# Kernel optimization log

Hardware: AMD Instinct MI355X
Metric: run time of the kernel (lower is better)

## Reference

```python
import jax, jax.numpy as jnp
import numpy as np


def _hard_sigmoid(x):
    # Keras ConvLSTM2D default recurrent_activation
    return jnp.clip(0.2 * x + 0.5, 0.0, 1.0)


def _conv(x, w):
    # NHWC input, HWIO kernel, SAME padding, stride 1
    return jax.lax.conv_general_dilated(
        x, w, (1, 1), 'SAME', dimension_numbers=('NHWC', 'HWIO', 'NHWC'))


def _convlstm(seq, h, c, k, rk, b):
    # seq: [B, T, H, W, Cin]; h, c: [B, H, W, F]
    # k: [kh, kw, Cin, 4F], rk: [kh, kw, F, 4F], b: [4F]
    def step(carry, x):
        h, c = carry
        z = _conv(x, k) + _conv(h, rk) + b  # [B,H,W,4F]
        zi, zf, zc, zo = jnp.split(z, 4, axis=-1)
        i = _hard_sigmoid(zi)
        f = _hard_sigmoid(zf)
        o = _hard_sigmoid(zo)
        c = f * c + i * jnp.tanh(zc)
        h = o * jnp.tanh(c)
        return (h, c), None
    (h, c), _ = jax.lax.scan(step, (h, c), jnp.swapaxes(seq, 0, 1))
    return h, c


def setup_inputs() -> dict:
    key = jax.random.key(0)
    ks = jax.random.split(key, 14)
    B, T, H, W, Cin, F, K = 32, 1, 64, 64, 1, 64, 3
    s = 0.05
    inp = {
        'input_': jax.random.normal(ks[0], (B, T, H, W, Cin), jnp.float32),
        'h0': jax.random.normal(ks[1], (B, H, W, F), jnp.float32) * s,
        'c0': jax.random.normal(ks[2], (B, H, W, F), jnp.float32) * s,
        'h1': jax.random.normal(ks[3], (B, H, W, F), jnp.float32) * s,
        'c1': jax.random.normal(ks[4], (B, H, W, F), jnp.float32) * s,
        'k0': jax.random.normal(ks[5], (K, K, Cin, 4 * F), jnp.float32) * s,
        'rk0': jax.random.normal(ks[6], (K, K, F, 4 * F), jnp.float32) * s,
        'b0': jnp.zeros((4 * F,), jnp.float32),
        'k1': jax.random.normal(ks[7], (K, K, F, 4 * F), jnp.float32) * s,
        'rk1': jax.random.normal(ks[8], (K, K, F, 4 * F), jnp.float32) * s,
        'b1': jnp.zeros((4 * F,), jnp.float32),
        'cw': jax.random.normal(ks[9], (1, 1, F, 1), jnp.float32) * s,
        'cb': jnp.zeros((1,), jnp.float32),
    }
    return inp


def reference(input_, h0, c0, h1, c1, k0, rk0, b0, k1, rk1, b1, cw, cb):
    # Layer 0 consumes the input frame sequence (T=1)
    h0n, c0n = _convlstm(input_, h0, c0, k0, rk0, b0)
    # Layer 1 consumes layer-0's last hidden state as its (length-1) input
    h1n, c1n = _convlstm(h0n[:, None], h1, c1, k1, rk1, b1)
    frames = _conv(h1n, cw) + cb  # 1x1 conv head -> [B,H,W,1]
    return frames, h0n, c0n, h1n, c1n
```

## Files before the change

### kernel.cpp

```cpp
#include <hip/hip_runtime.h>
#include <hip/hip_bf16.h>

typedef short s16;
typedef __attribute__((ext_vector_type(8))) short bf16x8;
typedef __attribute__((ext_vector_type(4))) float f32x4;

__device__ __forceinline__ s16 f2bf(float f) {
  unsigned u = __builtin_bit_cast(unsigned, f);
  unsigned r = (u + 0x7FFFu + ((u >> 16) & 1u)) >> 16;
  return (s16)r;
}

__device__ __forceinline__ float hsig(float x) {
  return fminf(fmaxf(0.2f * x + 0.5f, 0.0f), 1.0f);
}

#define PXS 66
#define ROWSZ (PXS * 64)
#define ASZ4 (4 * ROWSZ)
#define ASZ6 (6 * ROWSZ)

__global__ void wprep_kernel(const float* __restrict__ rk0, const float* __restrict__ k1,
                             const float* __restrict__ rk1, const float* __restrict__ k0,
                             s16* __restrict__ w0q, s16* __restrict__ w1q,
                             s16* __restrict__ w2q, s16* __restrict__ k0t) {
  int idx = blockIdx.x * 256 + threadIdx.x;
  const int n1 = 18 * 8192;
  if (idx < 3 * n1) {
    int which = idx / n1;
    int i = idx - which * n1;
    int e    = i & 7;
    int lane = (i >> 3) & 63;
    int g    = (i >> 9) & 3;
    int j    = (i >> 11) & 3;
    int k    = (i >> 13) & 1;
    int tap  = i >> 14;
    int l15 = lane & 15, l4 = lane >> 4;
    int ic = k * 32 + l4 * 8 + e;
    int oc = j * 64 + g * 16 + l15;
    const float* src = (which == 0) ? rk0 : (which == 1) ? k1 : rk1;
    s16* dst = (which == 0) ? w0q : (which == 1) ? w1q : w2q;
    dst[i] = f2bf(src[(tap * 64 + ic) * 256 + oc]);
  } else if (idx < 3 * n1 + 8192) {
    int r = idx - 3 * n1;
    int kk = r & 31;
    int oc = r >> 5;
    k0t[r] = (kk < 9) ? f2bf(k0[kk * 256 + oc]) : (s16)0;
  }
}

template <bool F32>
__device__ __forceinline__ bf16x8 load_conv8(const void* src, long off) {
  if constexpr (F32) {
    const float* p = (const float*)src + off;
    float4 v0 = *reinterpret_cast<const float4*>(p);
    float4 v1 = *reinterpret_cast<const float4*>(p + 4);
    bf16x8 r;
    r[0] = f2bf(v0.x); r[1] = f2bf(v0.y); r[2] = f2bf(v0.z); r[3] = f2bf(v0.w);
    r[4] = f2bf(v1.x); r[5] = f2bf(v1.y); r[6] = f2bf(v1.z); r[7] = f2bf(v1.w);
    return r;
  } else {
    return *reinterpret_cast<const bf16x8*>((const s16*)src + off);
  }
}

template <bool F32, int ROWS, int NT>
__device__ __forceinline__ void stageA(s16* a_lds, const void* src, int b, int y0, int tid) {
  #pragma unroll
  for (int i = 0; i < ROWS * 512 / NT; ++i) {
    int c   = tid + i * NT;
    int row = c >> 9;
    int px  = (c >> 3) & 63;
    int cb  = c & 7;
    int y   = y0 - 1 + row;
    int xp  = px + 1;
    bf16x8 v = {};
    if ((unsigned)y < 64u)
      v = load_conv8<F32>(src, ((long)(b * 64 + y) * 64 + px) * 64 + cb * 8);
    *reinterpret_cast<bf16x8*>(a_lds + (row * PXS + xp) * 64 + ((cb ^ (xp & 7)) * 8)) = v;
  }
  if (tid < ROWS * 16) {
    int row = tid >> 4;
    int xp  = ((tid >> 3) & 1) ? 65 : 0;
    int cb  = tid & 7;
    bf16x8 z = {};
    *reinterpret_cast<bf16x8*>(a_lds + (row * PXS + xp) * 64 + cb * 8) = z;
  }
}

__global__ __launch_bounds__(1024, 4) void cell0_kernel(
    const float* __restrict__ h0,
    const s16* __restrict__ w0,
    const float* __restrict__ xin,
    const s16* __restrict__ k0t,
    const float* __restrict__ bias,
    const float* __restrict__ c_old,
    float* __restrict__ h_out,
    float* __restrict__ c_out,
    s16* __restrict__ hb_out)
{
  __shared__ __align__(16) s16 a_lds[ASZ4];
  __shared__ __align__(16) s16 w_lds[4][8192];
  __shared__ float x_lds[256];

  const int tid = threadIdx.x;
  const int b  = blockIdx.x >> 5;
  const int y0 = (blockIdx.x & 31) << 1;

  const int wave = tid >> 6;
  const int lane = tid & 63;
  const int g    = wave & 3;
  const int mq   = wave >> 2;
  const int l15  = lane & 15;
  const int l4   = lane >> 4;

  constexpr int NST = 18;

  auto issueW = [&](int u) {
    int v = (u >= NST) ? u - NST : u;
    const s16* wt = w0 + v * 8192;
    char* base = (char*)(&w_lds[0][0]) + (u & 3) * 16384 + (tid >> 6) * 1024;
    __builtin_amdgcn_global_load_lds(
        (const __attribute__((address_space(1))) void*)(wt + tid * 8),
        (__attribute__((address_space(3))) void*)base, 16, 0, 0);
  };
  auto readWf = [&](bf16x8 (&wf)[4], int u) {
    const s16* wb = &w_lds[u & 3][0] + g * 512 + lane * 8;
    #pragma unroll
    for (int j = 0; j < 4; ++j)
      wf[j] = *reinterpret_cast<const bf16x8*>(wb + j * 2048);
  };
  auto readA = [&](bf16x8 (&af)[2], int u) {
    int v = (u >= NST) ? u - NST : u;
    int tap = v >> 1, kk = v & 1;
    int dy = tap / 3, dx = tap - dy * 3;
    const char* sb = (const char*)a_lds + ((mq >> 1) + dy) * (ROWSZ * 2);
    #pragma unroll
    for (int m = 0; m < 2; ++m) {
      int xq   = (mq & 1) * 32 + m * 16 + l15 + dx;
      int boff = xq * 128 + ((((kk << 2) | l4) ^ (xq & 7)) << 4);
      af[m] = *reinterpret_cast<const bf16x8*>(sb + boff);
    }
  };

  f32x4 acc[2][4] = {};

  auto doMfma = [&](const bf16x8 (&af)[2], const bf16x8 (&wf)[4]) {
    __builtin_amdgcn_s_setprio(1);
    #pragma unroll
    for (int m = 0; m < 2; ++m) {
      #pragma unroll
      for (int j = 0; j < 4; ++j)
        acc[m][j] = __builtin_amdgcn_mfma_f32_16x16x32_bf16(af[m], wf[j], acc[m][j], 0, 0, 0);
    }
    __builtin_amdgcn_s_setprio(0);
  };

  issueW(0);
  issueW(1);
  issueW(2);
  stageA<true, 4, 1024>(a_lds, h0, b, y0, tid);
  if (tid < 256) {
    int row = tid >> 6, px = tid & 63;
    int y = y0 - 1 + row;
    x_lds[tid] = ((unsigned)y < 64u) ? xin[(b * 64 + y) * 64 + px] : 0.0f;
  }
  __syncthreads();

  {
    const int rb = mq >> 1;
    #pragma unroll
    for (int m = 0; m < 2; ++m) {
      int px = (mq & 1) * 32 + m * 16 + l15;
      bf16x8 ax = {};
      #pragma unroll
      for (int e = 0; e < 8; ++e) {
        int t = l4 * 8 + e;
        if (t < 9) {
          int dyt = t / 3, dxt = t - dyt * 3;
          int xx = px + dxt - 1;
          float xv = ((unsigned)xx < 64u) ? x_lds[(rb + dyt) * 64 + xx] : 0.0f;
          ax[e] = f2bf(xv);
        }
      }
      #pragma unroll
      for (int j = 0; j < 4; ++j) {
        int oc = j * 64 + g * 16 + l15;
        bf16x8 bx = *reinterpret_cast<const bf16x8*>(k0t + oc * 32 + l4 * 8);
        acc[m][j] = __builtin_amdgcn_mfma_f32_16x16x32_bf16(ax, bx, acc[m][j], 0, 0, 0);
      }
    }
  }

  bf16x8 afA[2], afB[2], wfA[4], wfB[4];
  readA(afA, 0);
  readWf(wfA, 0);
  #pragma unroll
  for (int u = 0; u < NST; u += 2) {
    asm volatile("s_waitcnt vmcnt(1)" ::: "memory");
    __builtin_amdgcn_s_barrier();
    issueW(u + 3);
    readA(afB, u + 1);
    readWf(wfB, u + 1);
    doMfma(afA, wfA);
    asm volatile("s_waitcnt vmcnt(1)" ::: "memory");
    __builtin_amdgcn_s_barrier();
    issueW(u + 4);
    readA(afA, u + 2);
    readWf(wfA, u + 2);
    doMfma(afB, wfB);
  }

  float bi[4];
  #pragma unroll
  for (int j = 0; j < 4; ++j) bi[j] = bias[j * 64 + g * 16 + l15];
  const int pix_base = b * 4096 + y0 * 64;
  const int f = g * 16 + l15;
  #pragma unroll
  for (int m = 0; m < 2; ++m) {
    #pragma unroll
    for (int r = 0; r < 4; ++r) {
      int pl = mq * 32 + m * 16 + l4 * 4 + r;
      int off = (pix_base + pl) * 64 + f;
      float zi = acc[m][0][r] + bi[0];
      float zf = acc[m][1][r] + bi[1];
      float zc = acc[m][2][r] + bi[2];
      float zo = acc[m][3][r] + bi[3];
      float ig = hsig(zi), fg = hsig(zf), og = hsig(zo);
      float cn = fg * c_old[off] + ig * tanhf(zc);
      float hn = og * tanhf(cn);
      c_out[off] = cn;
      h_out[off] = hn;
      hb_out[off] = f2bf(hn);
    }
  }
}

__global__ __launch_bounds__(512, 2) void cell1_kernel(
    const s16* __restrict__ src0,
    const float* __restrict__ src1,
    const s16* __restrict__ w0,
    const s16* __restrict__ w1,
    const float* __restrict__ bias,
    const float* __restrict__ c_old,
    float* __restrict__ h_out,
    float* __restrict__ c_out)
{
  __shared__ __align__(16) s16 a_lds[2 * ASZ6];
  __shared__ __align__(16) s16 w_lds[3][8192];

  const int tid = threadIdx.x;
  const int b  = blockIdx.x >> 4;
  const int y0 = (blockIdx.x & 15) << 2;

  const int wave = tid >> 6;
  const int lane = tid & 63;
  const int g    = wave & 3;
  const int mh   = wave >> 2;
  const int l15  = lane & 15;
  const int l4   = lane >> 4;

  constexpr int NST = 36;

  auto issueW = [&](int u) {
    int v = (u >= NST) ? u - NST : u;
    int si = (v >= 18) ? 1 : 0;
    const s16* wt = (si ? w1 : w0) + (v - 18 * si) * 8192;
    char* sl = (char*)(&w_lds[0][0]) + (u % 3) * 16384 + wave * 1024;
    __builtin_amdgcn_global_load_lds(
        (const __attribute__((address_space(1))) void*)(wt + wave * 512 + lane * 8),
        (__attribute__((address_space(3))) void*)sl, 16, 0, 0);
    __builtin_amdgcn_global_load_lds(
        (const __attribute__((address_space(1))) void*)(wt + 4096 + wave * 512 + lane * 8),
        (__attribute__((address_space(3))) void*)(sl + 8192), 16, 0, 0);
  };

  auto readWf = [&](bf16x8 (&wf)[4], int u) {
    const s16* wb = &w_lds[0][0] + (u % 3) * 8192 + g * 512 + lane * 8;
    #pragma unroll
    for (int j = 0; j < 4; ++j)
      wf[j] = *reinterpret_cast<const bf16x8*>(wb + j * 2048);
  };

  f32x4 acc[8][4] = {};

  auto doStage = [&](const bf16x8 (&wf)[4], int u) {
    int si = (u >= 18) ? 1 : 0;
    int uu = u - 18 * si;
    int tap = uu >> 1, kk = uu & 1;
    int dy = tap / 3, dx = tap - dy * 3;
    const char* sb = (const char*)a_lds + si * (ASZ6 * 2);
    bf16x8 af[8];
    #pragma unroll
    for (int m = 0; m < 8; ++m) {
      int row  = 2 * mh + (m >> 2) + dy;
      int xq   = (m & 3) * 16 + l15 + dx;
      int boff = xq * 128 + ((((kk << 2) | l4) ^ (xq & 7)) << 4);
      af[m] = *reinterpret_cast<const bf16x8*>(sb + row * (ROWSZ * 2) + boff);
    }
    __builtin_amdgcn_s_setprio(1);
    #pragma unroll
    for (int m = 0; m < 8; ++m) {
      #pragma unroll
      for (int j = 0; j < 4; ++j)
        acc[m][j] = __builtin_amdgcn_mfma_f32_16x16x32_bf16(af[m], wf[j], acc[m][j], 0, 0, 0);
    }
    __builtin_amdgcn_s_setprio(0);
  };

  issueW(0);
  issueW(1);
  stageA<false, 6, 512>(a_lds, src0, b, y0, tid);
  stageA<true, 6, 512>(a_lds + ASZ6, src1, b, y0, tid);
  __syncthreads();

  bf16x8 wfA[4], wfB[4];
  readWf(wfA, 0);
  #pragma unroll
  for (int u = 0; u < NST; u += 2) {
    asm volatile("s_waitcnt vmcnt(0)" ::: "memory");
    __builtin_amdgcn_s_barrier();
    issueW(u + 2);
    readWf(wfB, u + 1);
    doStage(wfA, u);
    asm volatile("s_waitcnt vmcnt(0)" ::: "memory");
    __builtin_amdgcn_s_barrier();
    issueW(u + 3);
    readWf(wfA, (u + 2 < NST) ? u + 2 : 0);
    doStage(wfB, u + 1);
  }

  float bi[4];
  #pragma unroll
  for (int j = 0; j < 4; ++j) bi[j] = bias[j * 64 + g * 16 + l15];
  const int pix_base = b * 4096 + y0 * 64;
  const int f = g * 16 + l15;
  #pragma unroll
  for (int m = 0; m < 8; ++m) {
    #pragma unroll
    for (int r = 0; r < 4; ++r) {
      int pl = (2 * mh + (m >> 2)) * 64 + (m & 3) * 16 + l4 * 4 + r;
      int off = (pix_base + pl) * 64 + f;
      float zi = acc[m][0][r] + bi[0];
      float zf = acc[m][1][r] + bi[1];
      float zc = acc[m][2][r] + bi[2];
      float zo = acc[m][3][r] + bi[3];
      float ig = hsig(zi), fg = hsig(zf), og = hsig(zo);
      float cn = fg * c_old[off] + ig * tanhf(zc);
      float hn = og * tanhf(cn);
      c_out[off] = cn;
      h_out[off] = hn;
    }
  }
}

__global__ void frames_kernel(const float* __restrict__ h, const float* __restrict__ cw,
                              const float* __restrict__ cbp, float* __restrict__ out) {
  int tid = blockIdx.x * 256 + threadIdx.x;
  int p  = tid >> 2;
  int fc = (tid & 3) * 16;
  const float4* hp = reinterpret_cast<const float4*>(h + p * 64 + fc);
  const float4* wp = reinterpret_cast<const float4*>(cw + fc);
  float s = 0.0f;
  #pragma unroll
  for (int i = 0; i < 4; ++i) {
    float4 v = hp[i];
    float4 w = wp[i];
    s += v.x * w.x + v.y * w.y + v.z * w.z + v.w * w.w;
  }
  s += __shfl_xor(s, 1);
  s += __shfl_xor(s, 2);
  if ((tid & 3) == 0) out[p] = s + cbp[0];
}

extern "C" void kernel_launch(void* const* d_in, const int* in_sizes, int n_in,
                              void* d_out, int out_size, void* d_ws, size_t ws_size,
                              hipStream_t stream) {
  const float* x   = (const float*)d_in[0];
  const float* h0  = (const float*)d_in[1];
  const float* c0  = (const float*)d_in[2];
  const float* h1  = (const float*)d_in[3];
  const float* c1  = (const float*)d_in[4];
  const float* k0  = (const float*)d_in[5];
  const float* rk0 = (const float*)d_in[6];
  const float* b0  = (const float*)d_in[7];
  const float* k1  = (const float*)d_in[8];
  const float* rk1 = (const float*)d_in[9];
  const float* b1  = (const float*)d_in[10];
  const float* cw  = (const float*)d_in[11];
  const float* cbp = (const float*)d_in[12];

  float* out    = (float*)d_out;
  float* frames = out;
  float* h0n    = out + 131072;
  float* c0n    = out + 131072 + 8388608;
  float* h1n    = out + 131072 + 2 * 8388608;
  float* c1n    = out + 131072 + 3 * 8388608;

  char* ws = (char*)d_ws;
  const size_t SZ_H = 16777216;
  s16* h0nb = (s16*)(ws + 0 * SZ_H);
  s16* w0q  = (s16*)(ws + 1 * SZ_H);
  s16* w1q  = (s16*)(ws + 1 * SZ_H + 1 * 294912);
  s16* w2q  = (s16*)(ws + 1 * SZ_H + 2 * 294912);
  s16* k0t  = (s16*)(ws + 1 * SZ_H + 3 * 294912);

  wprep_kernel<<<1760, 256, 0, stream>>>(rk0, k1, rk1, k0, w0q, w1q, w2q, k0t);

  cell0_kernel<<<1024, 1024, 0, stream>>>(
      h0, w0q, x, k0t, b0, c0, h0n, c0n, h0nb);

  cell1_kernel<<<512, 512, 0, stream>>>(
      h0nb, h1, w1q, w2q, b1, c1, h1n, c1n);

  frames_kernel<<<2048, 256, 0, stream>>>(h1n, cw, cbp, frames);
}
```

Before: 202.6 us.

## Swap tile shapes between cell0 and cell1 kernels

Cell0 now processes four output rows per block with 512 blocks and a 3-slot weight ring, loading each weight stage once per larger tile. Cell1 switches to two rows per 1024-thread block with 1024 blocks and a 4-slot ring, trading weight reuse for more parallelism and occupancy. The goal is to rebalance per-kernel reuse against occupancy. In exchange, cell0 loads more redundant halo rows per block and cell1 refetches its weights from global memory twice as often.

```diff
diff --git a/kernel.cpp b/kernel.cpp
--- a/kernel.cpp
+++ b/kernel.cpp
@@ -88,7 +88,7 @@
   }
 }
 
-__global__ __launch_bounds__(1024, 4) void cell0_kernel(
+__global__ __launch_bounds__(1024, 1) void cell0_kernel(
     const float* __restrict__ h0,
     const s16* __restrict__ w0,
     const float* __restrict__ xin,
@@ -99,18 +99,18 @@
     float* __restrict__ c_out,
     s16* __restrict__ hb_out)
 {
-  __shared__ __align__(16) s16 a_lds[ASZ4];
-  __shared__ __align__(16) s16 w_lds[4][8192];
-  __shared__ float x_lds[256];
+  __shared__ __align__(16) s16 a_lds[ASZ6];
+  __shared__ __align__(16) s16 w_lds[3][8192];
+  __shared__ float x_lds[384];
 
   const int tid = threadIdx.x;
-  const int b  = blockIdx.x >> 5;
-  const int y0 = (blockIdx.x & 31) << 1;
+  const int b  = blockIdx.x >> 4;
+  const int y0 = (blockIdx.x & 15) << 2;
 
   const int wave = tid >> 6;
   const int lane = tid & 63;
   const int g    = wave & 3;
-  const int mq   = wave >> 2;
+  const int mh   = wave >> 2;
   const int l15  = lane & 15;
   const int l4   = lane >> 4;
 
@@ -119,36 +119,34 @@
   auto issueW = [&](int u) {
     int v = (u >= NST) ? u - NST : u;
     const s16* wt = w0 + v * 8192;
-    char* base = (char*)(&w_lds[0][0]) + (u & 3) * 16384 + (tid >> 6) * 1024;
+    char* base = (char*)(&w_lds[0][0]) + (v % 3) * 16384 + (tid >> 6) * 1024;
     __builtin_amdgcn_global_load_lds(
         (const __attribute__((address_space(1))) void*)(wt + tid * 8),
         (__attribute__((address_space(3))) void*)base, 16, 0, 0);
   };
-  auto readWf = [&](bf16x8 (&wf)[4], int u) {
-    const s16* wb = &w_lds[u & 3][0] + g * 512 + lane * 8;
+  auto readWf = [&](bf16x8 (&wf)[4], int slot) {
+    const s16* wb = &w_lds[slot][0] + g * 512 + lane * 8;
     #pragma unroll
     for (int j = 0; j < 4; ++j)
       wf[j] = *reinterpret_cast<const bf16x8*>(wb + j * 2048);
   };
-  auto readA = [&](bf16x8 (&af)[2], int u) {
-    int v = (u >= NST) ? u - NST : u;
-    int tap = v >> 1, kk = v & 1;
+
+  f32x4 acc[4][4] = {};
+
+  auto doStage = [&](const bf16x8 (&wf)[4], int u) {
+    int tap = u >> 1, kk = u & 1;
     int dy = tap / 3, dx = tap - dy * 3;
-    const char* sb = (const char*)a_lds + ((mq >> 1) + dy) * (ROWSZ * 2);
-    #pragma unroll
-    for (int m = 0; m < 2; ++m) {
-      int xq   = (mq & 1) * 32 + m * 16 + l15 + dx;
+    const char* sb = (const char*)a_lds + (mh + dy) * (ROWSZ * 2);
+    bf16x8 af[4];
+    #pragma unroll
+    for (int m = 0; m < 4; ++m) {
+      int xq   = m * 16 + l15 + dx;
       int boff = xq * 128 + ((((kk << 2) | l4) ^ (xq & 7)) << 4);
       af[m] = *reinterpret_cast<const bf16x8*>(sb + boff);
     }
-  };
-
-  f32x4 acc[2][4] = {};
-
-  auto doMfma = [&](const bf16x8 (&af)[2], const bf16x8 (&wf)[4]) {
     __builtin_amdgcn_s_setprio(1);
     #pragma unroll
-    for (int m = 0; m < 2; ++m) {
+    for (int m = 0; m < 4; ++m) {
       #pragma unroll
       for (int j = 0; j < 4; ++j)
         acc[m][j] = __builtin_amdgcn_mfma_f32_16x16x32_bf16(af[m], wf[j], acc[m][j], 0, 0, 0);
@@ -158,9 +156,8 @@
 
   issueW(0);
   issueW(1);
-  issueW(2);
-  stageA<true, 4, 1024>(a_lds, h0, b, y0, tid);
-  if (tid < 256) {
+  stageA<true, 6, 1024>(a_lds, h0, b, y0, tid);
+  if (tid < 384) {
     int row = tid >> 6, px = tid & 63;
     int y = y0 - 1 + row;
     x_lds[tid] = ((unsigned)y < 64u) ? xin[(b * 64 + y) * 64 + px] : 0.0f;
@@ -168,10 +165,15 @@
   __syncthreads();
 
   {
-    const int rb = mq >> 1;
-    #pragma unroll
-    for (int m = 0; m < 2; ++m) {
-      int px = (mq & 1) * 32 + m * 16 + l15;
+    bf16x8 bx[4];
+    #pragma unroll
+    for (int j = 0; j < 4; ++j) {
+      int oc = j * 64 + g * 16 + l15;
+      bx[j] = *reinterpret_cast<const bf16x8*>(k0t + oc * 32 + l4 * 8);
+    }
+    #pragma unroll
+    for (int m = 0; m < 4; ++m) {
+      int px = m * 16 + l15;
       bf16x8 ax = {};
       #pragma unroll
       for (int e = 0; e < 8; ++e) {
@@ -179,18 +181,129 @@
         if (t < 9) {
           int dyt = t / 3, dxt = t - dyt * 3;
           int xx = px + dxt - 1;
-          float xv = ((unsigned)xx < 64u) ? x_lds[(rb + dyt) * 64 + xx] : 0.0f;
+          float xv = ((unsigned)xx < 64u) ? x_lds[(mh + dyt) * 64 + xx] : 0.0f;
           ax[e] = f2bf(xv);
         }
       }
       #pragma unroll
-      for (int j = 0; j < 4; ++j) {
-        int oc = j * 64 + g * 16 + l15;
-        bf16x8 bx = *reinterpret_cast<const bf16x8*>(k0t + oc * 32 + l4 * 8);
-        acc[m][j] = __builtin_amdgcn_mfma_f32_16x16x32_bf16(ax, bx, acc[m][j], 0, 0, 0);
-      }
-    }
-  }
+      for (int j = 0; j < 4; ++j)
+        acc[m][j] = __builtin_amdgcn_mfma_f32_16x16x32_bf16(ax, bx[j], acc[m][j], 0, 0, 0);
+    }
+  }
+
+  bf16x8 wf[4];
+  #pragma unroll
+  for (int u = 0; u < NST; ++u) {
+    asm volatile("s_waitcnt vmcnt(1)" ::: "memory");
+    __builtin_amdgcn_s_barrier();
+    __builtin_amdgcn_sched_barrier(0);
+    issueW(u + 2);
+    readWf(wf, u % 3);
+    doStage(wf, u);
+  }
+
+  float bi[4];
+  #pragma unroll
+  for (int j = 0; j < 4; ++j) bi[j] = bias[j * 64 + g * 16 + l15];
+  const int pix_base = b * 4096 + y0 * 64;
+  const int f = g * 16 + l15;
+  #pragma unroll
+  for (int m = 0; m < 4; ++m) {
+    #pragma unroll
+    for (int r = 0; r < 4; ++r) {
+      int pl = mh * 64 + m * 16 + l4 * 4 + r;
+      int off = (pix_base + pl) * 64 + f;
+      float zi = acc[m][0][r] + bi[0];
+      float zf = acc[m][1][r] + bi[1];
+      float zc = acc[m][2][r] + bi[2];
+      float zo = acc[m][3][r] + bi[3];
+      float ig = hsig(zi), fg = hsig(zf), og = hsig(zo);
+      float cn = fg * c_old[off] + ig * tanhf(zc);
+      float hn = og * tanhf(cn);
+      c_out[off] = cn;
+      h_out[off] = hn;
+      hb_out[off] = f2bf(hn);
+    }
+  }
+}
+
+__global__ __launch_bounds__(1024, 4) void cell1_kernel(
+    const s16* __restrict__ src0,
+    const float* __restrict__ src1,
+    const s16* __restrict__ w0,
+    const s16* __restrict__ w1,
+    const float* __restrict__ bias,
+    const float* __restrict__ c_old,
+    float* __restrict__ h_out,
+    float* __restrict__ c_out)
+{
+  __shared__ __align__(16) s16 a_lds[2 * ASZ4];
+  __shared__ __align__(16) s16 w_lds[4][8192];
+
+  const int tid = threadIdx.x;
+  const int b  = blockIdx.x >> 5;
+  const int y0 = (blockIdx.x & 31) << 1;
+
+  const int wave = tid >> 6;
+  const int lane = tid & 63;
+  const int g    = wave & 3;
+  const int mq   = wave >> 2;
+  const int l15  = lane & 15;
+  const int l4   = lane >> 4;
+
+  constexpr int NST = 36;
+
+  auto issueW = [&](int u) {
+    int v = (u >= NST) ? u - NST : u;
+    int si = (v >= 18) ? 1 : 0;
+    const s16* wt = (si ? w1 : w0) + (v - 18 * si) * 8192;
+    char* base = (char*)(&w_lds[0][0]) + (u & 3) * 16384 + (tid >> 6) * 1024;
+    __builtin_amdgcn_global_load_lds(
+        (const __attribute__((address_space(1))) void*)(wt + tid * 8),
+        (__attribute__((address_space(3))) void*)base, 16, 0, 0);
+  };
+
+  auto readWf = [&](bf16x8 (&wf)[4], int u) {
+    const s16* wb = &w_lds[u & 3][0] + g * 512 + lane * 8;
+    #pragma unroll
+    for (int j = 0; j < 4; ++j)
+      wf[j] = *reinterpret_cast<const bf16x8*>(wb + j * 2048);
+  };
+
+  auto readA = [&](bf16x8 (&af)[2], int u) {
+    int v = (u >= NST) ? u - NST : u;
+    int si = (v >= 18) ? 1 : 0;
+    int uu = v - 18 * si;
+    int tap = uu >> 1, kk = uu & 1;
+    int dy = tap / 3, dx = tap - dy * 3;
+    const char* sb = (const char*)a_lds + si * (ASZ4 * 2) + ((mq >> 1) + dy) * (ROWSZ * 2);
+    #pragma unroll
+    for (int m = 0; m < 2; ++m) {
+      int xq   = (mq & 1) * 32 + m * 16 + l15 + dx;
+      int boff = xq * 128 + ((((kk << 2) | l4) ^ (xq & 7)) << 4);
+      af[m] = *reinterpret_cast<const bf16x8*>(sb + boff);
+    }
+  };
+
+  f32x4 acc[2][4] = {};
+
+  auto doMfma = [&](const bf16x8 (&af)[2], const bf16x8 (&wf)[4]) {
+    __builtin_amdgcn_s_setprio(1);
+    #pragma unroll
+    for (int m = 0; m < 2; ++m) {
+      #pragma unroll
+      for (int j = 0; j < 4; ++j)
+        acc[m][j] = __builtin_amdgcn_mfma_f32_16x16x32_bf16(af[m], wf[j], acc[m][j], 0, 0, 0);
+    }
+    __builtin_amdgcn_s_setprio(0);
+  };
+
+  issueW(0);
+  issueW(1);
+  issueW(2);
+  stageA<false, 4, 1024>(a_lds, src0, b, y0, tid);
+  stageA<true, 4, 1024>(a_lds + ASZ4, src1, b, y0, tid);
+  __syncthreads();
 
   bf16x8 afA[2], afB[2], wfA[4], wfB[4];
   readA(afA, 0);
@@ -221,125 +334,6 @@
     #pragma unroll
     for (int r = 0; r < 4; ++r) {
       int pl = mq * 32 + m * 16 + l4 * 4 + r;
-      int off = (pix_base + pl) * 64 + f;
-      float zi = acc[m][0][r] + bi[0];
-      float zf = acc[m][1][r] + bi[1];
-      float zc = acc[m][2][r] + bi[2];
-      float zo = acc[m][3][r] + bi[3];
-      float ig = hsig(zi), fg = hsig(zf), og = hsig(zo);
-      float cn = fg * c_old[off] + ig * tanhf(zc);
-      float hn = og * tanhf(cn);
-      c_out[off] = cn;
-      h_out[off] = hn;
-      hb_out[off] = f2bf(hn);
-    }
-  }
-}
-
-__global__ __launch_bounds__(512, 2) void cell1_kernel(
-    const s16* __restrict__ src0,
-    const float* __restrict__ src1,
-    const s16* __restrict__ w0,
-    const s16* __restrict__ w1,
-    const float* __restrict__ bias,
-    const float* __restrict__ c_old,
-    float* __restrict__ h_out,
-    float* __restrict__ c_out)
-{
-  __shared__ __align__(16) s16 a_lds[2 * ASZ6];
-  __shared__ __align__(16) s16 w_lds[3][8192];
-
-  const int tid = threadIdx.x;
-  const int b  = blockIdx.x >> 4;
-  const int y0 = (blockIdx.x & 15) << 2;
-
-  const int wave = tid >> 6;
-  const int lane = tid & 63;
-  const int g    = wave & 3;
-  const int mh   = wave >> 2;
-  const int l15  = lane & 15;
-  const int l4   = lane >> 4;
-
-  constexpr int NST = 36;
-
-  auto issueW = [&](int u) {
-    int v = (u >= NST) ? u - NST : u;
-    int si = (v >= 18) ? 1 : 0;
-    const s16* wt = (si ? w1 : w0) + (v - 18 * si) * 8192;
-    char* sl = (char*)(&w_lds[0][0]) + (u % 3) * 16384 + wave * 1024;
-    __builtin_amdgcn_global_load_lds(
-        (const __attribute__((address_space(1))) void*)(wt + wave * 512 + lane * 8),
-        (__attribute__((address_space(3))) void*)sl, 16, 0, 0);
-    __builtin_amdgcn_global_load_lds(
-        (const __attribute__((address_space(1))) void*)(wt + 4096 + wave * 512 + lane * 8),
-        (__attribute__((address_space(3))) void*)(sl + 8192), 16, 0, 0);
-  };
-
-  auto readWf = [&](bf16x8 (&wf)[4], int u) {
-    const s16* wb = &w_lds[0][0] + (u % 3) * 8192 + g * 512 + lane * 8;
-    #pragma unroll
-    for (int j = 0; j < 4; ++j)
-      wf[j] = *reinterpret_cast<const bf16x8*>(wb + j * 2048);
-  };
-
-  f32x4 acc[8][4] = {};
-
-  auto doStage = [&](const bf16x8 (&wf)[4], int u) {
-    int si = (u >= 18) ? 1 : 0;
-    int uu = u - 18 * si;
-    int tap = uu >> 1, kk = uu & 1;
-    int dy = tap / 3, dx = tap - dy * 3;
-    const char* sb = (const char*)a_lds + si * (ASZ6 * 2);
-    bf16x8 af[8];
-    #pragma unroll
-    for (int m = 0; m < 8; ++m) {
-      int row  = 2 * mh + (m >> 2) + dy;
-      int xq   = (m & 3) * 16 + l15 + dx;
-      int boff = xq * 128 + ((((kk << 2) | l4) ^ (xq & 7)) << 4);
-      af[m] = *reinterpret_cast<const bf16x8*>(sb + row * (ROWSZ * 2) + boff);
-    }
-    __builtin_amdgcn_s_setprio(1);
-    #pragma unroll
-    for (int m = 0; m < 8; ++m) {
-      #pragma unroll
-      for (int j = 0; j < 4; ++j)
-        acc[m][j] = __builtin_amdgcn_mfma_f32_16x16x32_bf16(af[m], wf[j], acc[m][j], 0, 0, 0);
-    }
-    __builtin_amdgcn_s_setprio(0);
-  };
-
-  issueW(0);
-  issueW(1);
-  stageA<false, 6, 512>(a_lds, src0, b, y0, tid);
-  stageA<true, 6, 512>(a_lds + ASZ6, src1, b, y0, tid);
-  __syncthreads();
-
-  bf16x8 wfA[4], wfB[4];
-  readWf(wfA, 0);
-  #pragma unroll
-  for (int u = 0; u < NST; u += 2) {
-    asm volatile("s_waitcnt vmcnt(0)" ::: "memory");
-    __builtin_amdgcn_s_barrier();
-    issueW(u + 2);
-    readWf(wfB, u + 1);
-    doStage(wfA, u);
-    asm volatile("s_waitcnt vmcnt(0)" ::: "memory");
-    __builtin_amdgcn_s_barrier();
-    issueW(u + 3);
-    readWf(wfA, (u + 2 < NST) ? u + 2 : 0);
-    doStage(wfB, u + 1);
-  }
-
-  float bi[4];
-  #pragma unroll
-  for (int j = 0; j < 4; ++j) bi[j] = bias[j * 64 + g * 16 + l15];
-  const int pix_base = b * 4096 + y0 * 64;
-  const int f = g * 16 + l15;
-  #pragma unroll
-  for (int m = 0; m < 8; ++m) {
-    #pragma unroll
-    for (int r = 0; r < 4; ++r) {
-      int pl = (2 * mh + (m >> 2)) * 64 + (m & 3) * 16 + l4 * 4 + r;
       int off = (pix_base + pl) * 64 + f;
       float zi = acc[m][0][r] + bi[0];
       float zf = acc[m][1][r] + bi[1];
@@ -407,10 +401,10 @@
 
   wprep_kernel<<<1760, 256, 0, stream>>>(rk0, k1, rk1, k0, w0q, w1q, w2q, k0t);
 
-  cell0_kernel<<<1024, 1024, 0, stream>>>(
+  cell0_kernel<<<512, 1024, 0, stream>>>(
       h0, w0q, x, k0t, b0, c0, h0n, c0n, h0nb);
 
-  cell1_kernel<<<512, 512, 0, stream>>>(
+  cell1_kernel<<<1024, 1024, 0, stream>>>(
       h0nb, h1, w1q, w2q, b1, c1, h1n, c1n);
 
   frames_kernel<<<2048, 256, 0, stream>>>(h1n, cw, cbp, frames);
```

Measured after the change: 182.2 us. -10.1%, faster.
